# Kernel optimization log

Measured on AMD Instinct MI355X. Metric: run time of the kernel, lower is better.

## Reference

```python
import jax, jax.numpy as jnp
import numpy as np

B, T, D = 2, 2048, 2048
HQ, HKV, HD = 16, 8, 128
GROUP = HQ // HKV
EPS = 1e-6


def rms_norm(x, scale):
    # qwen3-compatible: compute in fp32
    xf = x.astype(jnp.float32)
    var = jnp.mean(xf * xf, axis=-1, keepdims=True)
    return (xf * jax.lax.rsqrt(var + EPS) * scale).astype(x.dtype)


def apply_rope(x, cos, sin):
    # x: [B,H,T,d]; cos,sin: [T,d]
    d2 = x.shape[-1] // 2
    x1, x2 = x[..., :d2], x[..., d2:]
    rot = jnp.concatenate([-x2, x1], axis=-1)
    return (x * cos[None, None] + rot * sin[None, None]).astype(x.dtype)


def setup_inputs() -> dict:
    key = jax.random.key(0)
    ks = jax.random.split(key, 8)
    x = jax.random.normal(ks[0], (B, T, D), dtype=jnp.float32)
    # causal mask: True where attention is disallowed (j > i)
    mask = jnp.triu(jnp.ones((T, T), dtype=jnp.bool_), k=1)
    # RoPE tables
    inv_freq = 1.0 / (10000.0 ** (np.arange(0, HD, 2, dtype=np.float32) / HD))
    pos = np.arange(T, dtype=np.float32)
    ang = np.outer(pos, inv_freq)  # [T, HD/2]
    ang = np.concatenate([ang, ang], axis=-1)  # [T, HD]
    cos = jnp.asarray(np.cos(ang), dtype=jnp.float32)
    sin = jnp.asarray(np.sin(ang), dtype=jnp.float32)
    s = 0.02
    Wq = jax.random.normal(ks[1], (HQ * HD, D), dtype=jnp.float32) * s
    Wk = jax.random.normal(ks[2], (HKV * HD, D), dtype=jnp.float32) * s
    Wv = jax.random.normal(ks[3], (HKV * HD, D), dtype=jnp.float32) * s
    Wo = jax.random.normal(ks[4], (D, HQ * HD), dtype=jnp.float32) * s
    q_scale = jnp.ones((HD,), dtype=jnp.float32)
    k_scale = jnp.ones((HD,), dtype=jnp.float32)
    return {"x": x, "mask": mask, "cos": cos, "sin": sin,
            "Wq": Wq, "Wk": Wk, "Wv": Wv, "Wo": Wo,
            "q_scale": q_scale, "k_scale": k_scale}


def reference(x, mask, cos, sin, Wq, Wk, Wv, Wo, q_scale, k_scale):
    Bc, Tc, _ = x.shape
    Q = jnp.einsum('btd,ed->bte', x, Wq).reshape(Bc, Tc, HQ, HD).transpose(0, 2, 1, 3)
    K = jnp.einsum('btd,ed->bte', x, Wk).reshape(Bc, Tc, HKV, HD).transpose(0, 2, 1, 3)
    V = jnp.einsum('btd,ed->bte', x, Wv).reshape(Bc, Tc, HKV, HD).transpose(0, 2, 1, 3)
    Q = rms_norm(Q, q_scale)
    K = rms_norm(K, k_scale)
    Q = apply_rope(Q, cos, sin)
    K = apply_rope(K, cos, sin)
    K = jnp.repeat(K, GROUP, axis=1)  # [B,HQ,T,d]
    V = jnp.repeat(V, GROUP, axis=1)
    S = jnp.einsum('bhqd,bhkd->bhqk', Q, K) / jnp.sqrt(jnp.float32(HD))
    S = jnp.where(mask[None, None], -jnp.inf, S)
    P = jax.nn.softmax(S, axis=-1)
    ctx = jnp.einsum('bhqk,bhkd->bhqd', P, V).transpose(0, 2, 1, 3).reshape(Bc, Tc, HQ * HD)
    return jnp.einsum('bte,de->btd', ctx, Wo)
```

## Files before the change

kernel.cpp:

```cpp
#include <hip/hip_runtime.h>
#include <cstdint>
#include <cstddef>

#define B_ 2
#define T_ 2048
#define D_ 2048
#define HQ_ 16
#define HKV_ 8
#define HD_ 128

typedef __attribute__((ext_vector_type(8))) short short8;
typedef __attribute__((ext_vector_type(8))) unsigned short ushort8;
typedef __attribute__((ext_vector_type(4))) float f32x4;
typedef __attribute__((ext_vector_type(2))) unsigned short ushort2v;
typedef __attribute__((ext_vector_type(4))) unsigned short ushort4v;
typedef __attribute__((ext_vector_type(2))) float float2v;
typedef __attribute__((ext_vector_type(4))) float float4v;

__device__ __forceinline__ unsigned short f2bf(float f) {
  unsigned int u = __builtin_bit_cast(unsigned int, f);
  u += 0x7fffu + ((u >> 16) & 1u);
  return (unsigned short)(u >> 16);
}
__device__ __forceinline__ float bf2f(unsigned short h) {
  unsigned int u = ((unsigned int)h) << 16;
  return __builtin_bit_cast(float, u);
}

#if defined(__has_builtin)
#if __has_builtin(__builtin_amdgcn_global_load_lds)
#define HAS_GLL 1
#endif
#endif
#ifndef HAS_GLL
#define HAS_GLL 0
#endif

__device__ __forceinline__ void gll16(const void* g, void* l) {
#if HAS_GLL
  __builtin_amdgcn_global_load_lds((const __attribute__((address_space(1))) void*)g,
                                   (__attribute__((address_space(3))) void*)l, 16, 0, 0);
#else
  *(ushort8*)((char*)l + (threadIdx.x & 63) * 16) = *(const ushort8*)g;
#endif
}

__global__ __launch_bounds__(256) void cast_all(const float* __restrict__ x,
                                                const float* __restrict__ wq,
                                                const float* __restrict__ wk,
                                                const float* __restrict__ wv,
                                                const float* __restrict__ wo,
                                                unsigned short* __restrict__ xb,
                                                unsigned short* __restrict__ wqkv,
                                                unsigned short* __restrict__ wob) {
  const int base = blockIdx.x * 4096;
  const float* s;
  unsigned short* d;
  int soff, doff;
  if (base < 8388608)       { s = x;  soff = base;            d = xb;   doff = base; }
  else if (base < 12582912) { s = wq; soff = base - 8388608;  d = wqkv; doff = base - 8388608; }
  else if (base < 14680064) { s = wk; soff = base - 12582912; d = wqkv; doff = base - 8388608; }
  else if (base < 16777216) { s = wv; soff = base - 14680064; d = wqkv; doff = base - 8388608; }
  else                      { s = wo; soff = base - 16777216; d = wob;  doff = base - 16777216; }
#pragma unroll
  for (int k = 0; k < 4; k++) {
    const int off = (k * 256 + threadIdx.x) * 4;
    float4v v = *(const float4v*)(s + soff + off);
    ushort4v o; o.x = f2bf(v.x); o.y = f2bf(v.y); o.z = f2bf(v.z); o.w = f2bf(v.w);
    *(ushort4v*)(d + doff + off) = o;
  }
}

#define PH_SYNC { __builtin_amdgcn_s_barrier(); \
                  asm volatile("s_waitcnt lgkmcnt(0)" ::: "memory"); \
                  __builtin_amdgcn_sched_barrier(0); \
                  __builtin_amdgcn_s_setprio(1); }
#define PH_END  { __builtin_amdgcn_s_setprio(0); \
                  __builtin_amdgcn_s_barrier(); \
                  __builtin_amdgcn_sched_barrier(0); }

#define LDA(BUF, QM) { \
  _Pragma("unroll") for (int ii = 0; ii < BM/64; ii++) { \
    _Pragma("unroll") for (int ks = 0; ks < 2; ks++) \
      a[ii][ks] = *(const short8*)&Abuf[BUF][((QM)*(BM/2) + wm*(BM/4) + ii*16 + c)*64 + (((ks*4+g)^cs)*8)]; } }

#define LDB(BUF, QN, BB) { \
  _Pragma("unroll") for (int jj = 0; jj < 2; jj++) { \
    _Pragma("unroll") for (int ks = 0; ks < 2; ks++) \
      BB[jj][ks] = *(const short8*)&Bbuf[BUF][((QN)*128 + wn*32 + jj*16 + c)*64 + (((ks*4+g)^cs)*8)]; } }

#define MM(QM, QN, BB) { \
  _Pragma("unroll") for (int ii = 0; ii < BM/64; ii++) { \
    _Pragma("unroll") for (int jj = 0; jj < 2; jj++) { \
      f32x4 t_ = __builtin_amdgcn_mfma_f32_16x16x32_bf16(a[ii][0], BB[jj][0], acc[(QM)*(BM/64)+ii][(QN)*2+jj], 0, 0, 0); \
      acc[(QM)*(BM/64)+ii][(QN)*2+jj] = __builtin_amdgcn_mfma_f32_16x16x32_bf16(a[ii][1], BB[jj][1], t_, 0, 0, 0); } } }

template<int BM, int M, int N, int K, bool BF16_OUT>
__global__ __launch_bounds__(512, 2) void gemm8(const unsigned short* __restrict__ A,
                                                const unsigned short* __restrict__ W,
                                                void* __restrict__ Cout) {
  __shared__ __align__(16) unsigned short Abuf[2][BM * 64];
  __shared__ __align__(16) unsigned short Bbuf[2][256 * 64];
  const int tid = threadIdx.x;
  const int lane = tid & 63;
  const int wv = tid >> 6;
  const int g = lane >> 4;
  const int c = lane & 15;
  const int cs = c & 7;
  const int wm = wv >> 2;
  const int wn = wv & 3;

  constexpr int SH_Q = (BM == 256) ? 7 : 6;
  constexpr int SH_W = SH_Q - 1;

  constexpr int NT = N / 256;
  constexpr int NWG = (M / BM) * NT;
  constexpr int CHUNK = NWG / 8;
  const int bid = blockIdx.x;
  const int swz = (bid & 7) * CHUNK + (bid >> 3);
  const int m0 = (swz / NT) * BM;
  const int n0 = (swz % NT) * 256;

  const int prl = wv * 8 + (lane >> 3);
  const int scl = lane & 7;
#define STA(BUF, P0, KO) { \
    int pr_ = (P0) + prl; \
    int lr_ = ((pr_ >> SH_W) & 1) * (BM/2) + ((pr_ >> SH_Q) & 1) * (BM/4) + (pr_ & (BM/4 - 1)); \
    int lc_ = (scl ^ (pr_ & 7)) * 8; \
    gll16(&A[(size_t)(m0 + lr_) * K + (KO) + lc_], &Abuf[BUF][(P0) * 64 + wv * 512]); }
#define STB(BUF, P0, KO) { \
    int pr_ = (P0) + prl; \
    int lr_ = ((pr_ >> 5) & 3) * 64 + ((pr_ >> 7) & 1) * 32 + (pr_ & 31); \
    int lc_ = (scl ^ (pr_ & 7)) * 8; \
    gll16(&W[(size_t)(n0 + lr_) * K + (KO) + lc_], &Bbuf[BUF][(P0) * 64 + wv * 512]); }

#define STAGE_PH2(BUF, KO) { if constexpr (BM == 256) { STA(BUF, 0, KO); STA(BUF, 64, KO); } \
                             else { STA(BUF, 0, KO); } \
                             STB(BUF, 0, KO); STB(BUF, 64, KO); }
#define STAGE_PH3(BUF, KO) { STB(BUF, 128, KO); STB(BUF, 192, KO); }
#define STAGE_PH4(BUF, KO) { if constexpr (BM == 256) { STA(BUF, 128, KO); STA(BUF, 192, KO); } \
                             else { STA(BUF, 64, KO); } }
#define VMW { if constexpr (BM == 256) { asm volatile("s_waitcnt vmcnt(8)" ::: "memory"); } \
              else { asm volatile("s_waitcnt vmcnt(6)" ::: "memory"); } }

  short8 a[BM/64][2], b0[2][2], b1[2][2];
  f32x4 acc[BM/32][4];
#pragma unroll
  for (int i = 0; i < BM/32; i++)
#pragma unroll
    for (int j = 0; j < 4; j++) acc[i][j] = (f32x4)0.0f;

  STAGE_PH2(0, 0); STAGE_PH3(0, 0); STAGE_PH4(0, 0);
  STAGE_PH2(1, 64); STAGE_PH3(1, 64); STAGE_PH4(1, 64);
  VMW;
  __builtin_amdgcn_s_barrier();

  constexpr int NITER = K / 128;
  for (int it = 0; it < NITER - 1; ++it) {
    const int k2 = it * 128 + 128;
    const int k3 = k2 + 64;
    LDA(0, 0); LDB(0, 0, b0);
    PH_SYNC; MM(0, 0, b0); PH_END;
    LDB(0, 1, b1);
    STAGE_PH2(0, k2);
    PH_SYNC; MM(0, 1, b1); PH_END;
    LDA(0, 1);
    STAGE_PH3(0, k2);
    PH_SYNC; MM(1, 1, b1); PH_END;
    STAGE_PH4(0, k2);
    VMW;
    PH_SYNC; MM(1, 0, b0); PH_END;
    LDA(1, 0); LDB(1, 0, b0);
    PH_SYNC; MM(0, 0, b0); PH_END;
    LDB(1, 1, b1);
    STAGE_PH2(1, k3);
    PH_SYNC; MM(0, 1, b1); PH_END;
    LDA(1, 1);
    STAGE_PH3(1, k3);
    PH_SYNC; MM(1, 1, b1); PH_END;
    STAGE_PH4(1, k3);
    VMW;
    PH_SYNC; MM(1, 0, b0); PH_END;
  }
  LDA(0, 0); LDB(0, 0, b0); PH_SYNC; MM(0, 0, b0); PH_END;
  LDB(0, 1, b1);            PH_SYNC; MM(0, 1, b1); PH_END;
  LDA(0, 1);                PH_SYNC; MM(1, 1, b1); PH_END;
  asm volatile("s_waitcnt vmcnt(0)" ::: "memory");
  PH_SYNC; MM(1, 0, b0); PH_END;
  LDA(1, 0); LDB(1, 0, b0); PH_SYNC; MM(0, 0, b0); PH_END;
  LDB(1, 1, b1);            PH_SYNC; MM(0, 1, b1); PH_END;
  LDA(1, 1);                PH_SYNC; MM(1, 1, b1); PH_END;
  PH_SYNC; MM(1, 0, b0); PH_END;

#pragma unroll
  for (int I = 0; I < BM/32; I++)
#pragma unroll
    for (int J = 0; J < 4; J++)
#pragma unroll
      for (int r = 0; r < 4; r++) {
        int row = m0 + wm * (BM/2) + I * 16 + g * 4 + r;
        int col = n0 + wn * 64 + J * 16 + c;
        if (BF16_OUT)
          ((unsigned short*)Cout)[(size_t)row * N + col] = f2bf(acc[I][J][r]);
        else
          ((float*)Cout)[(size_t)row * N + col] = acc[I][J][r];
      }
#undef STA
#undef STB
#undef STAGE_PH2
#undef STAGE_PH3
#undef STAGE_PH4
#undef VMW
}

__global__ __launch_bounds__(256) void rope_and_vt(const unsigned short* __restrict__ qkv,
                                                   const float* __restrict__ cosT,
                                                   const float* __restrict__ sinT,
                                                   const float* __restrict__ q_scale,
                                                   const float* __restrict__ k_scale,
                                                   unsigned short* __restrict__ Qb,
                                                   unsigned short* __restrict__ Kb,
                                                   unsigned short* __restrict__ Vt) {
  __shared__ unsigned short lds[128 * 65];
  const int tid = threadIdx.x;
  if (blockIdx.x < 4096) {
    const int lane = tid & 63;
    const int wvq = tid >> 6;
    const int row = blockIdx.x;
    const int b = row >> 11;
    const int t = row & 2047;
    const int d0 = lane * 2;

    const float2v cs = *(const float2v*)&cosT[t * 128 + d0];
    const float2v sn = *(const float2v*)&sinT[t * 128 + d0];
    const float2v qsc = *(const float2v*)&q_scale[d0];
    const float2v ksc = *(const float2v*)&k_scale[d0];
    const float sgn = (lane < 32) ? -1.0f : 1.0f;
    const unsigned short* base = qkv + (size_t)row * 4096;

#pragma unroll
    for (int s6 = 0; s6 < 6; s6++) {
      const int slot = wvq * 6 + s6;
      const bool isQ = slot < 16;
      const unsigned short* src = base + (isQ ? slot * 128 : 2048 + (slot - 16) * 128);
      ushort2v u = *(const ushort2v*)&src[d0];
      float x0 = bf2f(u.x), x1 = bf2f(u.y);
      float ss = x0 * x0 + x1 * x1;
      ss += __shfl_xor(ss, 1);  ss += __shfl_xor(ss, 2);  ss += __shfl_xor(ss, 4);
      ss += __shfl_xor(ss, 8);  ss += __shfl_xor(ss, 16); ss += __shfl_xor(ss, 32);
      float rinv = rsqrtf(ss * (1.0f / 128.0f) + 1e-6f);
      float2v scv = isQ ? qsc : ksc;
      float xn0 = x0 * rinv * scv.x;
      float xn1 = x1 * rinv * scv.y;
      float o0 = __shfl_xor(xn0, 32);
      float o1 = __shfl_xor(xn1, 32);
      float r0v = xn0 * cs.x + sgn * o0 * sn.x;
      float r1v = xn1 * cs.y + sgn * o1 * sn.y;
      ushort2v out; out.x = f2bf(r0v); out.y = f2bf(r1v);
      unsigned short* dst;
      if (isQ) dst = Qb + ((size_t)(b * HQ_ + slot) * T_ + t) * HD_;
      else     dst = Kb + ((size_t)(b * HKV_ + (slot - 16)) * T_ + t) * HD_;
      *(ushort2v*)&dst[d0] = out;
    }
  } else {
    const int blk = blockIdx.x - 4096;
    const int tblk = blk & 31;
    const int kv = (blk >> 5) & 7;
    const int b = blk >> 8;
    const int t0 = tblk * 64;
    const int r = tid >> 2;
    const int seg = tid & 3;
    const unsigned short* src = qkv + (size_t)(b * T_ + t0 + r) * 4096 + 3072 + kv * 128;
    for (int i = 0; i < 4; i++) {
      int cc = seg * 32 + i * 8;
      ushort8 v = *(const ushort8*)&src[cc];
      for (int q = 0; q < 8; q++) lds[(cc + q) * 65 + r] = v[q];
    }
    __syncthreads();
    const int cI = tid >> 1;
    const int rs = (tid & 1) * 32;
    unsigned short* dst = Vt + ((size_t)(b * HKV_ + kv) * HD_ + cI) * T_ + t0 + rs;
    const unsigned short* srow = &lds[cI * 65 + rs];
    for (int j = 0; j < 32; j += 4) {
      ushort4v v; v.x = srow[j]; v.y = srow[j + 1]; v.z = srow[j + 2]; v.w = srow[j + 3];
      *(ushort4v*)&dst[j] = v;
    }
  }
}

__global__ __launch_bounds__(256) void attn(const unsigned short* __restrict__ Qb,
                                            const unsigned short* __restrict__ Kb,
                                            const unsigned short* __restrict__ Vt,
                                            unsigned short* __restrict__ ctxb) {
  __shared__ __align__(16) unsigned short Ks[2][64 * 128];
  __shared__ __align__(16) unsigned short Vs[2][128 * 64];
  __shared__ __align__(16) unsigned short Ps[4][16 * 72];
  const int tid = threadIdx.x;
  const int lane = tid & 63;
  const int wv = tid >> 6;
  const int g = lane >> 4;
  const int c = lane & 15;

  const int blk = blockIdx.x;
  const int kv = blk & 7;
  const int idx = blk >> 3;
  const int p = idx >> 2;
  const int b = (idx >> 1) & 1;
  const int h = kv * 2 + (idx & 1);

  const unsigned short* Kh = Kb + (size_t)(b * HKV_ + kv) * T_ * HD_;
  const unsigned short* Vh = Vt + (size_t)(b * HKV_ + kv) * HD_ * T_;
  const float scale = 0.08838834764831845f;

#define STAGE_KV(BF, KT) { \
  _Pragma("unroll") for (int i_ = 0; i_ < 4; i_++) { \
    const int ch_ = wv * 256 + i_ * 64 + lane; \
    const int rK_ = ch_ >> 4, cK_ = ch_ & 15; \
    gll16(Kh + (size_t)((KT) * 64 + rK_) * HD_ + (cK_ ^ (rK_ & 7)) * 8, \
          Ks[BF] + (size_t)(wv * 256 + i_ * 64) * 8); \
    const int rV_ = ch_ >> 3, cV_ = ch_ & 7; \
    gll16(Vh + (size_t)rV_ * T_ + (KT) * 64 + (cV_ ^ (rV_ & 7)) * 8, \
          Vs[BF] + (size_t)(wv * 256 + i_ * 64) * 8); } }

  for (int ph = 0; ph < 2; ph++) {
    const int qb = ph ? (31 - p) : p;
    const int nkt = qb + 1;
    const unsigned short* Qh = Qb + ((size_t)(b * HQ_ + h) * T_ + qb * 64 + wv * 16) * HD_;

    short8 aq[4];
#pragma unroll
    for (int dk = 0; dk < 4; dk++) aq[dk] = *(const short8*)&Qh[c * HD_ + dk * 32 + g * 8];

    f32x4 acc[8];
#pragma unroll
    for (int dc = 0; dc < 8; dc++) acc[dc] = (f32x4)0.0f;
    float lp[4] = {0.0f, 0.0f, 0.0f, 0.0f};

    STAGE_KV(0, 0);
    __syncthreads();

    for (int kt = 0; kt < nkt; kt++) {
      const int cur = kt & 1;
      if (kt + 1 < nkt) { STAGE_KV(cur ^ 1, kt + 1); }
      __builtin_amdgcn_sched_barrier(0);

      f32x4 s[4];
#pragma unroll
      for (int kf = 0; kf < 4; kf++) s[kf] = (f32x4)0.0f;
      __builtin_amdgcn_s_setprio(1);
#pragma unroll
      for (int dk = 0; dk < 4; dk++) {
#pragma unroll
        for (int kf = 0; kf < 4; kf++) {
          short8 bk = *(const short8*)&Ks[cur][(kf * 16 + c) * 128 + ((dk * 4 + g) ^ (c & 7)) * 8];
          s[kf] = __builtin_amdgcn_mfma_f32_16x16x32_bf16(aq[dk], bk, s[kf], 0, 0, 0);
        }
      }
      __builtin_amdgcn_s_setprio(0);

      const bool diag = (kt == nkt - 1);
#pragma unroll
      for (int kf = 0; kf < 4; kf++) {
#pragma unroll
        for (int r = 0; r < 4; r++) {
          float pv = __expf(s[kf][r] * scale);
          if (diag) {
            int key = kt * 64 + kf * 16 + c;
            int rowq = qb * 64 + wv * 16 + g * 4 + r;
            if (key > rowq) pv = 0.0f;
          }
          lp[r] += pv;
          Ps[wv][(g * 4 + r) * 72 + kf * 16 + c] = f2bf(pv);
        }
      }

      short8 ap[2];
      ap[0] = *(const short8*)&Ps[wv][c * 72 + g * 8];
      ap[1] = *(const short8*)&Ps[wv][c * 72 + 32 + g * 8];
      __builtin_amdgcn_s_setprio(1);
#pragma unroll
      for (int dc = 0; dc < 8; dc++) {
#pragma unroll
        for (int kf2 = 0; kf2 < 2; kf2++) {
          short8 bv = *(const short8*)&Vs[cur][(dc * 16 + c) * 64 + ((kf2 * 4 + g) ^ (c & 7)) * 8];
          acc[dc] = __builtin_amdgcn_mfma_f32_16x16x32_bf16(ap[kf2], bv, acc[dc], 0, 0, 0);
        }
      }
      __builtin_amdgcn_s_setprio(0);

      __syncthreads();
    }

#pragma unroll
    for (int r = 0; r < 4; r++) {
      float l = lp[r];
      l += __shfl_xor(l, 1); l += __shfl_xor(l, 2);
      l += __shfl_xor(l, 4); l += __shfl_xor(l, 8);
      float inv = 1.0f / l;
      int row = b * T_ + qb * 64 + wv * 16 + g * 4 + r;
#pragma unroll
      for (int dc = 0; dc < 8; dc++)
        ctxb[(size_t)row * (HQ_ * HD_) + h * HD_ + dc * 16 + c] = f2bf(acc[dc][r] * inv);
    }
  }
#undef STAGE_KV
}

extern "C" void kernel_launch(void* const* d_in, const int* in_sizes, int n_in,
                              void* d_out, int out_size, void* d_ws, size_t ws_size,
                              hipStream_t stream) {
  const float* x = (const float*)d_in[0];
  const float* cosT = (const float*)d_in[2];
  const float* sinT = (const float*)d_in[3];
  const float* Wq = (const float*)d_in[4];
  const float* Wk = (const float*)d_in[5];
  const float* Wv = (const float*)d_in[6];
  const float* Wo = (const float*)d_in[7];
  const float* q_scale = (const float*)d_in[8];
  const float* k_scale = (const float*)d_in[9];

  char* ws = (char*)d_ws;
  unsigned short* qkv  = (unsigned short*)(ws + 0);
  unsigned short* ctxb = qkv;
  unsigned short* xb   = (unsigned short*)(ws + 33554432);
  unsigned short* wqkv = (unsigned short*)(ws + 50331648);
  unsigned short* wob  = (unsigned short*)(ws + 67108864);
  unsigned short* Qb   = (unsigned short*)(ws + 75497472);
  unsigned short* Kb   = (unsigned short*)(ws + 92274688);
  unsigned short* Vt   = (unsigned short*)(ws + 100663296);

  cast_all<<<5120, 256, 0, stream>>>(x, Wq, Wk, Wv, Wo, xb, wqkv, wob);
  gemm8<256, 4096, 4096, 2048, true><<<256, 512, 0, stream>>>(xb, wqkv, qkv);
  rope_and_vt<<<4608, 256, 0, stream>>>(qkv, cosT, sinT, q_scale, k_scale, Qb, Kb, Vt);
  attn<<<512, 256, 0, stream>>>(Qb, Kb, Vt, ctxb);
  gemm8<128, 4096, 2048, 2048, false><<<256, 512, 0, stream>>>(ctxb, wob, d_out);
}
```

Measured before the change: 326.2 us.

## Double-buffer register fragments to prefetch LDS reads under MFMA phases

Adds a second A register fragment set and rotates the A/B fragment buffers so that the LDS reads for the next MFMA phase are issued inside the current phase, overlapping them with the matrix instructions. This is meant to hide LDS read latency that previously sat on the critical path between phases. It costs extra VGPRs, which could spill or reduce occupancy under launch_bounds(512,2). The buffer rotation across phases and the loop boundary is intricate and could contain a hazard.

After: 376.5 us. 1.15x slower.

```diff
diff --git a/kernel.cpp b/kernel.cpp
--- a/kernel.cpp
+++ b/kernel.cpp
@@ -78,22 +78,23 @@
 #define PH_END  { __builtin_amdgcn_s_setprio(0); \
                   __builtin_amdgcn_s_barrier(); \
                   __builtin_amdgcn_sched_barrier(0); }
-
-#define LDA(BUF, QM) { \
+#define SBAR __builtin_amdgcn_sched_barrier(0)
+
+#define PREF_A(AA, BUF, QM) { \
   _Pragma("unroll") for (int ii = 0; ii < BM/64; ii++) { \
     _Pragma("unroll") for (int ks = 0; ks < 2; ks++) \
-      a[ii][ks] = *(const short8*)&Abuf[BUF][((QM)*(BM/2) + wm*(BM/4) + ii*16 + c)*64 + (((ks*4+g)^cs)*8)]; } }
-
-#define LDB(BUF, QN, BB) { \
+      AA[ii][ks] = *(const short8*)&Abuf[BUF][((QM)*(BM/2) + wm*(BM/4) + ii*16 + c)*64 + (((ks*4+g)^cs)*8)]; } }
+
+#define PREF_B(BB, BUF, QN) { \
   _Pragma("unroll") for (int jj = 0; jj < 2; jj++) { \
     _Pragma("unroll") for (int ks = 0; ks < 2; ks++) \
       BB[jj][ks] = *(const short8*)&Bbuf[BUF][((QN)*128 + wn*32 + jj*16 + c)*64 + (((ks*4+g)^cs)*8)]; } }
 
-#define MM(QM, QN, BB) { \
+#define MM(QM, QN, AA, BB) { \
   _Pragma("unroll") for (int ii = 0; ii < BM/64; ii++) { \
     _Pragma("unroll") for (int jj = 0; jj < 2; jj++) { \
-      f32x4 t_ = __builtin_amdgcn_mfma_f32_16x16x32_bf16(a[ii][0], BB[jj][0], acc[(QM)*(BM/64)+ii][(QN)*2+jj], 0, 0, 0); \
-      acc[(QM)*(BM/64)+ii][(QN)*2+jj] = __builtin_amdgcn_mfma_f32_16x16x32_bf16(a[ii][1], BB[jj][1], t_, 0, 0, 0); } } }
+      f32x4 t_ = __builtin_amdgcn_mfma_f32_16x16x32_bf16(AA[ii][0], BB[jj][0], acc[(QM)*(BM/64)+ii][(QN)*2+jj], 0, 0, 0); \
+      acc[(QM)*(BM/64)+ii][(QN)*2+jj] = __builtin_amdgcn_mfma_f32_16x16x32_bf16(AA[ii][1], BB[jj][1], t_, 0, 0, 0); } } }
 
 template<int BM, int M, int N, int K, bool BF16_OUT>
 __global__ __launch_bounds__(512, 2) void gemm8(const unsigned short* __restrict__ A,
@@ -143,7 +144,7 @@
 #define VMW { if constexpr (BM == 256) { asm volatile("s_waitcnt vmcnt(8)" ::: "memory"); } \
               else { asm volatile("s_waitcnt vmcnt(6)" ::: "memory"); } }
 
-  short8 a[BM/64][2], b0[2][2], b1[2][2];
+  short8 a0[BM/64][2], a1[BM/64][2], b0[2][2], b1[2][2];
   f32x4 acc[BM/32][4];
 #pragma unroll
   for (int i = 0; i < BM/32; i++)
@@ -154,43 +155,38 @@
   STAGE_PH2(1, 64); STAGE_PH3(1, 64); STAGE_PH4(1, 64);
   VMW;
   __builtin_amdgcn_s_barrier();
+  PREF_A(a0, 0, 0); PREF_B(b0, 0, 0);
 
   constexpr int NITER = K / 128;
   for (int it = 0; it < NITER - 1; ++it) {
     const int k2 = it * 128 + 128;
     const int k3 = k2 + 64;
-    LDA(0, 0); LDB(0, 0, b0);
-    PH_SYNC; MM(0, 0, b0); PH_END;
-    LDB(0, 1, b1);
+    PH_SYNC; PREF_B(b1, 0, 1); SBAR; MM(0, 0, a0, b0); PH_END;
     STAGE_PH2(0, k2);
-    PH_SYNC; MM(0, 1, b1); PH_END;
-    LDA(0, 1);
+    PH_SYNC; PREF_A(a1, 0, 1); SBAR; MM(0, 1, a0, b1); PH_END;
     STAGE_PH3(0, k2);
-    PH_SYNC; MM(1, 1, b1); PH_END;
+    PH_SYNC; MM(1, 1, a1, b1); PH_END;
     STAGE_PH4(0, k2);
     VMW;
-    PH_SYNC; MM(1, 0, b0); PH_END;
-    LDA(1, 0); LDB(1, 0, b0);
-    PH_SYNC; MM(0, 0, b0); PH_END;
-    LDB(1, 1, b1);
+    PH_SYNC; PREF_A(a0, 1, 0); PREF_B(b1, 1, 0); SBAR; MM(1, 0, a1, b0); PH_END;
+    PH_SYNC; PREF_B(b0, 1, 1); SBAR; MM(0, 0, a0, b1); PH_END;
     STAGE_PH2(1, k3);
-    PH_SYNC; MM(0, 1, b1); PH_END;
-    LDA(1, 1);
+    PH_SYNC; PREF_A(a1, 1, 1); SBAR; MM(0, 1, a0, b0); PH_END;
     STAGE_PH3(1, k3);
-    PH_SYNC; MM(1, 1, b1); PH_END;
+    PH_SYNC; MM(1, 1, a1, b0); PH_END;
     STAGE_PH4(1, k3);
     VMW;
-    PH_SYNC; MM(1, 0, b0); PH_END;
+    PH_SYNC; PREF_A(a0, 0, 0); PREF_B(b0, 0, 0); SBAR; MM(1, 0, a1, b1); PH_END;
   }
-  LDA(0, 0); LDB(0, 0, b0); PH_SYNC; MM(0, 0, b0); PH_END;
-  LDB(0, 1, b1);            PH_SYNC; MM(0, 1, b1); PH_END;
-  LDA(0, 1);                PH_SYNC; MM(1, 1, b1); PH_END;
+  PH_SYNC; PREF_B(b1, 0, 1); SBAR; MM(0, 0, a0, b0); PH_END;
+  PH_SYNC; PREF_A(a1, 0, 1); SBAR; MM(0, 1, a0, b1); PH_END;
+  PH_SYNC; MM(1, 1, a1, b1); PH_END;
   asm volatile("s_waitcnt vmcnt(0)" ::: "memory");
-  PH_SYNC; MM(1, 0, b0); PH_END;
-  LDA(1, 0); LDB(1, 0, b0); PH_SYNC; MM(0, 0, b0); PH_END;
-  LDB(1, 1, b1);            PH_SYNC; MM(0, 1, b1); PH_END;
-  LDA(1, 1);                PH_SYNC; MM(1, 1, b1); PH_END;
-  PH_SYNC; MM(1, 0, b0); PH_END;
+  PH_SYNC; PREF_A(a0, 1, 0); PREF_B(b1, 1, 0); SBAR; MM(1, 0, a1, b0); PH_END;
+  PH_SYNC; PREF_B(b0, 1, 1); SBAR; MM(0, 0, a0, b1); PH_END;
+  PH_SYNC; PREF_A(a1, 1, 1); SBAR; MM(0, 1, a0, b0); PH_END;
+  PH_SYNC; MM(1, 1, a1, b0); PH_END;
+  PH_SYNC; MM(1, 0, a1, b1); PH_END;
 
 #pragma unroll
   for (int I = 0; I < BM/32; I++)
```

## Add double-buffered two-workgroup-per-CU GEMM for output projection

Applied to the files above, without the earlier changes.

Introduces a new gemm2p kernel with a 128x256 tile, double-buffered LDS and launch bounds allowing two workgroups per CU, and uses it for the final Wo projection instead of gemm8. The schedule interleaves global-to-LDS loads with MFMA phases and uses vmcnt waits to overlap memory with compute. The goal is better latency hiding through occupancy. The cost is higher LDS use per block and fewer in-flight stages.

After: 332.6 us. About the same (+2.0%).

```diff
diff --git a/kernel.cpp b/kernel.cpp
--- a/kernel.cpp
+++ b/kernel.cpp
@@ -78,6 +78,7 @@
 #define PH_END  { __builtin_amdgcn_s_setprio(0); \
                   __builtin_amdgcn_s_barrier(); \
                   __builtin_amdgcn_sched_barrier(0); }
+#define SBAR __builtin_amdgcn_sched_barrier(0)
 
 #define LDA(BUF, QM) { \
   _Pragma("unroll") for (int ii = 0; ii < BM/64; ii++) { \
@@ -211,6 +212,123 @@
 #undef STAGE_PH3
 #undef STAGE_PH4
 #undef VMW
+}
+
+template<int M, int N, int K, bool BF16_OUT>
+__global__ __launch_bounds__(512, 2) void gemm2p(const unsigned short* __restrict__ A,
+                                                 const unsigned short* __restrict__ W,
+                                                 void* __restrict__ Cout) {
+  __shared__ __align__(16) unsigned short Abuf[2][128 * 64];
+  __shared__ __align__(16) unsigned short Bbuf[2][256 * 64];
+  const int tid = threadIdx.x;
+  const int lane = tid & 63;
+  const int wv = tid >> 6;
+  const int g = lane >> 4;
+  const int c = lane & 15;
+  const int cs = c & 7;
+  const int wm = wv >> 2;
+  const int wn = wv & 3;
+
+  constexpr int NT = N / 256;
+  constexpr int NWG = (M / 128) * NT;
+  constexpr int CHUNK = NWG / 8;
+  const int bid = blockIdx.x;
+  const int swz = (bid & 7) * CHUNK + (bid >> 3);
+  const int m0 = (swz / NT) * 128;
+  const int n0 = (swz % NT) * 256;
+
+  const int prl = wv * 8 + (lane >> 3);
+  const int scl = lane & 7;
+#define STA_P(BUF, P0, KO) { \
+    int pr_ = (P0) + prl; \
+    int lr_ = ((pr_ >> 5) & 1) * 64 + ((pr_ >> 6) & 1) * 32 + (pr_ & 31); \
+    int lc_ = (scl ^ (pr_ & 7)) * 8; \
+    gll16(&A[(size_t)(m0 + lr_) * K + (KO) + lc_], &Abuf[BUF][(P0) * 64 + wv * 512]); }
+#define STB_P(BUF, P0, KO) { \
+    int pr_ = (P0) + prl; \
+    int lr_ = ((pr_ >> 5) & 3) * 64 + ((pr_ >> 7) & 1) * 32 + (pr_ & 31); \
+    int lc_ = (scl ^ (pr_ & 7)) * 8; \
+    gll16(&W[(size_t)(n0 + lr_) * K + (KO) + lc_], &Bbuf[BUF][(P0) * 64 + wv * 512]); }
+#define STB4_P(BUF, KO) { STB_P(BUF, 0, KO); STB_P(BUF, 64, KO); STB_P(BUF, 128, KO); STB_P(BUF, 192, KO); }
+#define LDA_P(BUF, QM) { \
+    _Pragma("unroll") for (int ii = 0; ii < 2; ii++) { \
+      _Pragma("unroll") for (int ks = 0; ks < 2; ks++) \
+        a[ii][ks] = *(const short8*)&Abuf[BUF][((QM)*64 + wm*32 + ii*16 + c)*64 + (((ks*4+g)^cs)*8)]; } }
+#define LDB_P(BUF, QN, BB) { \
+    _Pragma("unroll") for (int jj = 0; jj < 2; jj++) { \
+      _Pragma("unroll") for (int ks = 0; ks < 2; ks++) \
+        BB[jj][ks] = *(const short8*)&Bbuf[BUF][((QN)*128 + wn*32 + jj*16 + c)*64 + (((ks*4+g)^cs)*8)]; } }
+#define MM_P(QM, QN, BB) { \
+    _Pragma("unroll") for (int ii = 0; ii < 2; ii++) { \
+      _Pragma("unroll") for (int jj = 0; jj < 2; jj++) { \
+        f32x4 t_ = __builtin_amdgcn_mfma_f32_16x16x32_bf16(a[ii][0], BB[jj][0], acc[(QM)*2+ii][(QN)*2+jj], 0, 0, 0); \
+        acc[(QM)*2+ii][(QN)*2+jj] = __builtin_amdgcn_mfma_f32_16x16x32_bf16(a[ii][1], BB[jj][1], t_, 0, 0, 0); } } }
+#define VMW5 { asm volatile("s_waitcnt vmcnt(5)" ::: "memory"); SBAR; }
+
+  short8 a[2][2], b0[2][2], b1[2][2];
+  f32x4 acc[4][4];
+#pragma unroll
+  for (int i = 0; i < 4; i++)
+#pragma unroll
+    for (int j = 0; j < 4; j++) acc[i][j] = (f32x4)0.0f;
+
+  STA_P(0, 0, 0); STA_P(0, 64, 0); STB4_P(0, 0);
+  STA_P(1, 0, 64); STB4_P(1, 64);
+  asm volatile("s_waitcnt vmcnt(5)" ::: "memory");
+  __builtin_amdgcn_s_barrier();
+
+  constexpr int NITER = K / 128;
+  for (int it = 0; it < NITER - 1; ++it) {
+    const int kB1 = it * 128 + 64;
+    const int kN0 = it * 128 + 128;
+    const int kN1 = it * 128 + 192;
+    VMW5;
+    STA_P(1, 64, kB1);
+    LDA_P(0, 0); LDB_P(0, 0, b0); LDB_P(0, 1, b1);
+    PH_SYNC; MM_P(0, 0, b0); MM_P(0, 1, b1); PH_END;
+    STA_P(0, 0, kN0); STB4_P(0, kN0);
+    LDA_P(0, 1);
+    PH_SYNC; MM_P(1, 1, b1); MM_P(1, 0, b0); PH_END;
+    VMW5;
+    STA_P(0, 64, kN0);
+    LDA_P(1, 0); LDB_P(1, 0, b0); LDB_P(1, 1, b1);
+    PH_SYNC; MM_P(0, 0, b0); MM_P(0, 1, b1); PH_END;
+    STA_P(1, 0, kN1); STB4_P(1, kN1);
+    LDA_P(1, 1);
+    PH_SYNC; MM_P(1, 1, b1); MM_P(1, 0, b0); PH_END;
+  }
+  VMW5;
+  STA_P(1, 64, (NITER - 1) * 128 + 64);
+  LDA_P(0, 0); LDB_P(0, 0, b0); LDB_P(0, 1, b1);
+  PH_SYNC; MM_P(0, 0, b0); MM_P(0, 1, b1); PH_END;
+  LDA_P(0, 1);
+  PH_SYNC; MM_P(1, 1, b1); MM_P(1, 0, b0); PH_END;
+  asm volatile("s_waitcnt vmcnt(0)" ::: "memory"); SBAR;
+  LDA_P(1, 0); LDB_P(1, 0, b0); LDB_P(1, 1, b1);
+  PH_SYNC; MM_P(0, 0, b0); MM_P(0, 1, b1); PH_END;
+  LDA_P(1, 1);
+  PH_SYNC; MM_P(1, 1, b1); MM_P(1, 0, b0); PH_END;
+
+#pragma unroll
+  for (int I = 0; I < 4; I++)
+#pragma unroll
+    for (int J = 0; J < 4; J++)
+#pragma unroll
+      for (int r = 0; r < 4; r++) {
+        int row = m0 + wm * 64 + I * 16 + g * 4 + r;
+        int col = n0 + wn * 64 + J * 16 + c;
+        if (BF16_OUT)
+          ((unsigned short*)Cout)[(size_t)row * N + col] = f2bf(acc[I][J][r]);
+        else
+          ((float*)Cout)[(size_t)row * N + col] = acc[I][J][r];
+      }
+#undef STA_P
+#undef STB_P
+#undef STB4_P
+#undef LDA_P
+#undef LDB_P
+#undef MM_P
+#undef VMW5
 }
 
 __global__ __launch_bounds__(256) void rope_and_vt(const unsigned short* __restrict__ qkv,
@@ -433,5 +551,5 @@
   gemm8<256, 4096, 4096, 2048, true><<<256, 512, 0, stream>>>(xb, wqkv, qkv);
   rope_and_vt<<<4608, 256, 0, stream>>>(qkv, cosT, sinT, q_scale, k_scale, Qb, Kb, Vt);
   attn<<<512, 256, 0, stream>>>(Qb, Kb, Vt, ctxb);
-  gemm8<128, 4096, 2048, 2048, false><<<256, 512, 0, stream>>>(ctxb, wob, d_out);
-}
+  gemm2p<4096, 2048, 2048, false><<<256, 512, 0, stream>>>(ctxb, wob, d_out);
+}
```
